# Performance work log

Measured on AMD Instinct MI355X. Metric: run time of the kernel, lower is better.

Reference implementation:

```python
import jax, jax.numpy as jnp
import numpy as np


def setup_inputs() -> dict:
    key = jax.random.key(0)
    ks = jax.random.split(key, 7)
    E = 768; CH = 3; PS = 16; B = 128; P = 196
    return {
        "x": jax.random.normal(ks[0], (B, P, E), dtype=jnp.float32),
        "We": jax.random.normal(ks[1], (CH * PS * PS, E), dtype=jnp.float32) * (1.0 / np.sqrt(E)),
        "be": jax.random.normal(ks[2], (CH * PS * PS,), dtype=jnp.float32) * 0.01,
        "filter_re": jax.random.normal(ks[3], (1, 1, 1, PS, PS), dtype=jnp.float32),
        "filter_im": jax.random.normal(ks[4], (1, 1, 1, PS, PS), dtype=jnp.float32),
        "Wd": jax.random.normal(ks[5], (E, CH * PS * PS), dtype=jnp.float32) * (1.0 / np.sqrt(CH * PS * PS)),
        "bd": jax.random.normal(ks[6], (E,), dtype=jnp.float32) * 0.01,
        "ch": 3,
        "patch_size": 16,
    }


def reference(x, We, be, filter_re, filter_im, Wd, bd, ch, patch_size):
    # encode: [b,p,E] -> [b,p,ch*ps*ps]
    h = jnp.einsum('bpe,ce->bpc', x, We) + be
    b, p, _ = h.shape
    h = h.reshape(b, p, ch, patch_size, patch_size)
    # batched 2D FFT over the two trailing patch dims
    hf = jnp.fft.fft2(h, axes=(-2, -1))
    filt = (filter_re + 1j * filter_im).astype(hf.dtype)  # [1,1,1,ps,ps]
    r = jnp.fft.ifft2(hf * filt, axes=(-2, -1))
    a = jnp.abs(r).reshape(b, p, ch * patch_size * patch_size)
    # decode: [b,p,ch*ps*ps] -> [b,p,E]
    return jnp.einsum('bpc,ec->bpe', a, Wd) + bd
```

## Files before the change

kernel.cpp:

```cpp
#include <hip/hip_runtime.h>

typedef short short8 __attribute__((ext_vector_type(8)));
typedef unsigned short ushort8 __attribute__((ext_vector_type(8)));
typedef float f32x4 __attribute__((ext_vector_type(4)));

__device__ __forceinline__ unsigned short f32_to_bf16(float f) {
  unsigned u = __float_as_uint(f);
  unsigned r = 0x7fffu + ((u >> 16) & 1u);
  return (unsigned short)((u + r) >> 16);
}

__global__ void cvt_f32_bf16(const float* __restrict__ s,
                             unsigned short* __restrict__ d, int n8) {
  int i = blockIdx.x * blockDim.x + threadIdx.x;
  if (i >= n8) return;
  const float4* sp = (const float4*)s;
  float4 a = sp[2 * i], b = sp[2 * i + 1];
  ushort8 o;
  o[0] = f32_to_bf16(a.x); o[1] = f32_to_bf16(a.y);
  o[2] = f32_to_bf16(a.z); o[3] = f32_to_bf16(a.w);
  o[4] = f32_to_bf16(b.x); o[5] = f32_to_bf16(b.y);
  o[6] = f32_to_bf16(b.z); o[7] = f32_to_bf16(b.w);
  ((ushort8*)d)[i] = o;
}

__device__ __forceinline__ void gload_lds16(const void* g, void* l) {
  auto* gp = (const __attribute__((address_space(1))) uint32_t*)((uintptr_t)g);
  auto* lp = (__attribute__((address_space(3))) uint32_t*)(uint32_t)(uintptr_t)l;
  __builtin_amdgcn_global_load_lds(gp, lp, 16, 0, 0);
}

constexpr float C16T[16] = {
    1.f,  0.9238795325112867f,  0.7071067811865476f,  0.3826834323650898f,
    0.f, -0.3826834323650898f, -0.7071067811865476f, -0.9238795325112867f,
   -1.f, -0.9238795325112867f, -0.7071067811865476f, -0.3826834323650898f,
    0.f,  0.3826834323650898f,  0.7071067811865476f,  0.9238795325112867f};
constexpr float S16T[16] = {
    0.f,  0.3826834323650898f,  0.7071067811865476f,  0.9238795325112867f,
    1.f,  0.9238795325112867f,  0.7071067811865476f,  0.3826834323650898f,
    0.f, -0.3826834323650898f, -0.7071067811865476f, -0.9238795325112867f,
   -1.f, -0.9238795325112867f, -0.7071067811865476f, -0.3826834323650898f};

__global__ __launch_bounds__(256) void build_gpp(
    const float* __restrict__ fre, const float* __restrict__ fim,
    unsigned short* __restrict__ Gpp) {
  __shared__ float Gr[256], Gi[256];
  const int t = threadIdx.x;
  const int d1 = t >> 4, d2 = t & 15;
  float sr = 0.f, si = 0.f;
#pragma unroll
  for (int v1 = 0; v1 < 16; ++v1) {
    const int k1 = (v1 * d1) & 15;
#pragma unroll
    for (int v2 = 0; v2 < 16; ++v2) {
      const int k = (k1 + v2 * d2) & 15;
      const float c = C16T[k], s = S16T[k];
      const float a = fre[v1 * 16 + v2], b = fim[v1 * 16 + v2];
      sr += a * c - b * s;
      si += a * s + b * c;
    }
  }
  Gr[t] = sr * (1.f / 256.f);
  Gi[t] = si * (1.f / 256.f);
  __syncthreads();
  const int p = blockIdx.x;
  const int p1 = p >> 4, p2 = p & 15;
  const size_t rre = (size_t)(p >> 5) * 64 + (p & 31);
  const int q1 = t >> 4, q2 = t & 15;
  const int idx = (((p1 - q1) & 15) << 4) | ((p2 - q2) & 15);
  Gpp[rre * 256 + t] = f32_to_bf16(Gr[idx]);
  Gpp[(rre + 32) * 256 + t] = f32_to_bf16(Gi[idx]);
}

template <int MODE>
__global__ __launch_bounds__(256, 5) void gemm32(
    const unsigned short* __restrict__ A, const unsigned short* __restrict__ B,
    const float* __restrict__ bias, void* __restrict__ out,
    int M, int K, int nbx, int ldo) {
  __shared__ __align__(16) unsigned short As[2][128 * 32];
  __shared__ __align__(16) unsigned short Bs[2][128 * 32];

  const int tid = threadIdx.x;
  const int lane = tid & 63;
  const int wid = tid >> 6;
  const int wr = wid >> 1, wc = wid & 1;

  const int nwg = gridDim.x;
  const int cpx = nwg >> 3;
  const int bid = blockIdx.x;
  const int lid = (bid & 7) * cpx + (bid >> 3);
  const int m0 = (lid / nbx) * 128, n0 = (lid % nbx) * 128;

  const int srow = tid >> 2;
  const int sgo = (((tid & 3) ^ ((tid >> 3) & 3)) << 3);
  char* AsC = (char*)&As[0][0];
  char* BsC = (char*)&Bs[0][0];

  auto STAGE = [&](int buf, int kt) {
    const int k0 = kt * 32 + sgo;
#pragma unroll
    for (int l = 0; l < 2; ++l) {
      gload_lds16(A + (size_t)(m0 + l * 64 + srow) * K + k0,
                  AsC + buf * 8192 + l * 4096 + (wid << 10));
      gload_lds16(B + (size_t)(n0 + l * 64 + srow) * K + k0,
                  BsC + buf * 8192 + l * 4096 + (wid << 10));
    }
  };

  const int rsel = lane & 15;
  const int kslot = ((lane >> 4) ^ ((lane >> 1) & 3)) << 4;

  f32x4 acc[4][4] = {};

  auto COMPUTE = [&](int buf) {
    const char* Ab = AsC + buf * 8192;
    const char* Bb = BsC + buf * 8192;
    short8 af[4], bf[4];
#pragma unroll
    for (int m = 0; m < 4; ++m)
      af[m] = *(const short8*)(Ab + (wr * 64 + m * 16 + rsel) * 64 + kslot);
#pragma unroll
    for (int n = 0; n < 4; ++n)
      bf[n] = *(const short8*)(Bb + (wc * 64 + n * 16 + rsel) * 64 + kslot);
#pragma unroll
    for (int m = 0; m < 4; ++m)
#pragma unroll
      for (int n = 0; n < 4; ++n)
        acc[m][n] = __builtin_amdgcn_mfma_f32_16x16x32_bf16(
            af[m], bf[n], acc[m][n], 0, 0, 0);
  };

  const int nk = K >> 5;
  STAGE(0, 0);
  __syncthreads();
  int cur = 0;
  for (int t = 1; t < nk; ++t) {
    STAGE(cur ^ 1, t);
    COMPUTE(cur);
    __syncthreads();
    cur ^= 1;
  }
  COMPUTE(cur);

  const int fr = lane & 15, fq = lane >> 4;
  if (MODE == 2) {
    const int cbase = (n0 + wc * 64) >> 1;
    unsigned short* o = (unsigned short*)out;
#pragma unroll
    for (int n = 0; n < 2; ++n) {
      const int gcol = cbase + n * 16 + fr;
#pragma unroll
      for (int m = 0; m < 4; ++m) {
        const int grow = m0 + wr * 64 + m * 16 + fq * 4;
#pragma unroll
        for (int j = 0; j < 4; ++j) {
          const float re = acc[m][n][j];
          const float im = acc[m][n + 2][j];
          o[(size_t)(grow + j) * ldo + gcol] =
              f32_to_bf16(sqrtf(re * re + im * im));
        }
      }
    }
  } else {
#pragma unroll
    for (int n = 0; n < 4; ++n) {
      const int gcol = n0 + wc * 64 + n * 16 + fr;
      const float bv = bias[gcol];
#pragma unroll
      for (int m = 0; m < 4; ++m) {
        const int grow = m0 + wr * 64 + m * 16 + fq * 4;
#pragma unroll
        for (int j = 0; j < 4; ++j) {
          const float v = acc[m][n][j] + bv;
          if (MODE == 1)
            ((unsigned short*)out)[(size_t)(grow + j) * ldo + gcol] =
                f32_to_bf16(v);
          else
            ((float*)out)[(size_t)(grow + j) * ldo + gcol] = v;
        }
      }
    }
  }
}

extern "C" void kernel_launch(void* const* d_in, const int* in_sizes, int n_in,
                              void* d_out, int out_size, void* d_ws,
                              size_t ws_size, hipStream_t stream) {
  const float* x   = (const float*)d_in[0];
  const float* We  = (const float*)d_in[1];
  const float* be  = (const float*)d_in[2];
  const float* fre = (const float*)d_in[3];
  const float* fim = (const float*)d_in[4];
  const float* Wd  = (const float*)d_in[5];
  const float* bd  = (const float*)d_in[6];

  const int E = 768, C = 768;
  const int nX = in_sizes[0];
  const int M  = nX / E;
  const int nW = E * C;

  char* w = (char*)d_ws;
  unsigned short* xb  = (unsigned short*)w;
  unsigned short* Web = (unsigned short*)(w + (size_t)nX * 2);
  unsigned short* Wdb = Web + nW;
  unsigned short* Gpp = Wdb + nW;
  unsigned short* hb  = Gpp + 512 * 256;

  cvt_f32_bf16<<<(nX / 8 + 255) / 256, 256, 0, stream>>>(x, xb, nX / 8);
  cvt_f32_bf16<<<(nW / 8 + 255) / 256, 256, 0, stream>>>(We, Web, nW / 8);
  cvt_f32_bf16<<<(nW / 8 + 255) / 256, 256, 0, stream>>>(Wd, Wdb, nW / 8);

  build_gpp<<<256, 256, 0, stream>>>(fre, fim, Gpp);

  gemm32<1><<<6 * (M / 128), 256, 0, stream>>>(xb, Web, be, hb, M, E, 6, 768);

  const int M2 = M * 3;
  gemm32<2><<<4 * (M2 / 128), 256, 0, stream>>>(hb, Gpp, nullptr, xb, M2, 256,
                                                4, 256);

  gemm32<0><<<6 * (M / 128), 256, 0, stream>>>(xb, Wdb, bd, (float*)d_out, M,
                                               C, 6, 768);
}
```

Before: 185.2 us.

## Deepen GEMM K-tile to 64 with vmcnt-based double-buffer pipeline

The shared GEMM kernel now stages 64-wide K tiles instead of 32, using an XOR swizzle on 128-byte LDS rows. The main loop now issues two stages up front and waits on vmcnt counts with raw barriers rather than __syncthreads, so global-to-LDS loads for tile t+2 overlap compute on tile t. The aim is fewer barriers per K step and more latency hiding. LDS use doubles to 64KB per block, and the launch-bounds occupancy hint is dropped, which may reduce resident blocks.

```diff
diff --git a/kernel.cpp b/kernel.cpp
--- a/kernel.cpp
+++ b/kernel.cpp
@@ -30,6 +30,20 @@
   __builtin_amdgcn_global_load_lds(gp, lp, 16, 0, 0);
 }
 
+#define WAIT8()                                        \
+  do {                                                 \
+    asm volatile("s_waitcnt vmcnt(8)" ::: "memory");   \
+  } while (0)
+#define WAIT0()                                        \
+  do {                                                 \
+    asm volatile("s_waitcnt vmcnt(0)" ::: "memory");   \
+  } while (0)
+#define BAR()                                          \
+  do {                                                 \
+    __builtin_amdgcn_s_barrier();                      \
+    __builtin_amdgcn_sched_barrier(0);                 \
+  } while (0)
+
 constexpr float C16T[16] = {
     1.f,  0.9238795325112867f,  0.7071067811865476f,  0.3826834323650898f,
     0.f, -0.3826834323650898f, -0.7071067811865476f, -0.9238795325112867f,
@@ -73,12 +87,12 @@
 }
 
 template <int MODE>
-__global__ __launch_bounds__(256, 5) void gemm32(
+__global__ __launch_bounds__(256) void gemm_cv(
     const unsigned short* __restrict__ A, const unsigned short* __restrict__ B,
     const float* __restrict__ bias, void* __restrict__ out,
     int M, int K, int nbx, int ldo) {
-  __shared__ __align__(16) unsigned short As[2][128 * 32];
-  __shared__ __align__(16) unsigned short Bs[2][128 * 32];
+  __shared__ __align__(16) unsigned short As[2][128 * 64];
+  __shared__ __align__(16) unsigned short Bs[2][128 * 64];
 
   const int tid = threadIdx.x;
   const int lane = tid & 63;
@@ -91,56 +105,59 @@
   const int lid = (bid & 7) * cpx + (bid >> 3);
   const int m0 = (lid / nbx) * 128, n0 = (lid % nbx) * 128;
 
-  const int srow = tid >> 2;
-  const int sgo = (((tid & 3) ^ ((tid >> 3) & 3)) << 3);
-  char* AsC = (char*)&As[0][0];
-  char* BsC = (char*)&Bs[0][0];
+  const int lr8 = lane >> 3;
+  const int swk = ((lane & 7) ^ lr8) * 8;
+
+  f32x4 acc[4][4] = {};
 
   auto STAGE = [&](int buf, int kt) {
-    const int k0 = kt * 32 + sgo;
-#pragma unroll
-    for (int l = 0; l < 2; ++l) {
-      gload_lds16(A + (size_t)(m0 + l * 64 + srow) * K + k0,
-                  AsC + buf * 8192 + l * 4096 + (wid << 10));
-      gload_lds16(B + (size_t)(n0 + l * 64 + srow) * K + k0,
-                  BsC + buf * 8192 + l * 4096 + (wid << 10));
+    const int k0 = kt * 64 + swk;
+#pragma unroll
+    for (int c = 0; c < 4; ++c) {
+      const int rowc = wid * 32 + c * 8;
+      gload_lds16(A + (size_t)(m0 + rowc + lr8) * K + k0, &As[buf][rowc * 64]);
+      gload_lds16(B + (size_t)(n0 + rowc + lr8) * K + k0, &Bs[buf][rowc * 64]);
     }
   };
 
   const int rsel = lane & 15;
-  const int kslot = ((lane >> 4) ^ ((lane >> 1) & 3)) << 4;
-
-  f32x4 acc[4][4] = {};
-
   auto COMPUTE = [&](int buf) {
-    const char* Ab = AsC + buf * 8192;
-    const char* Bb = BsC + buf * 8192;
-    short8 af[4], bf[4];
-#pragma unroll
-    for (int m = 0; m < 4; ++m)
-      af[m] = *(const short8*)(Ab + (wr * 64 + m * 16 + rsel) * 64 + kslot);
-#pragma unroll
-    for (int n = 0; n < 4; ++n)
-      bf[n] = *(const short8*)(Bb + (wc * 64 + n * 16 + rsel) * 64 + kslot);
-#pragma unroll
-    for (int m = 0; m < 4; ++m)
-#pragma unroll
-      for (int n = 0; n < 4; ++n)
-        acc[m][n] = __builtin_amdgcn_mfma_f32_16x16x32_bf16(
-            af[m], bf[n], acc[m][n], 0, 0, 0);
+#pragma unroll
+    for (int ks = 0; ks < 2; ++ks) {
+      const int kbyte = ks * 64 + (lane >> 4) * 16;
+      short8 af[4], bf[4];
+#pragma unroll
+      for (int m = 0; m < 4; ++m) {
+        const int row = wr * 64 + m * 16 + rsel;
+        af[m] = *(const short8*)((const char*)&As[buf][0] +
+                                 row * 128 + (kbyte ^ ((row & 7) << 4)));
+      }
+#pragma unroll
+      for (int n = 0; n < 4; ++n) {
+        const int row = wc * 64 + n * 16 + rsel;
+        bf[n] = *(const short8*)((const char*)&Bs[buf][0] +
+                                 row * 128 + (kbyte ^ ((row & 7) << 4)));
+      }
+#pragma unroll
+      for (int m = 0; m < 4; ++m)
+#pragma unroll
+        for (int n = 0; n < 4; ++n)
+          acc[m][n] = __builtin_amdgcn_mfma_f32_16x16x32_bf16(
+              af[m], bf[n], acc[m][n], 0, 0, 0);
+    }
   };
 
-  const int nk = K >> 5;
+  const int nk = K >> 6;
   STAGE(0, 0);
-  __syncthreads();
-  int cur = 0;
-  for (int t = 1; t < nk; ++t) {
-    STAGE(cur ^ 1, t);
-    COMPUTE(cur);
-    __syncthreads();
-    cur ^= 1;
+  STAGE(1, 1);
+  for (int t = 0; t < nk; ++t) {
+    if (t + 1 < nk) WAIT8();
+    else            WAIT0();
+    BAR();
+    COMPUTE(t & 1);
+    __builtin_amdgcn_s_barrier();
+    if (t + 2 < nk) STAGE(t & 1, t + 2);
   }
-  COMPUTE(cur);
 
   const int fr = lane & 15, fq = lane >> 4;
   if (MODE == 2) {
@@ -212,12 +229,12 @@
 
   build_gpp<<<256, 256, 0, stream>>>(fre, fim, Gpp);
 
-  gemm32<1><<<6 * (M / 128), 256, 0, stream>>>(xb, Web, be, hb, M, E, 6, 768);
+  gemm_cv<1><<<6 * (M / 128), 256, 0, stream>>>(xb, Web, be, hb, M, E, 6, 768);
 
   const int M2 = M * 3;
-  gemm32<2><<<4 * (M2 / 128), 256, 0, stream>>>(hb, Gpp, nullptr, xb, M2, 256,
-                                                4, 256);
-
-  gemm32<0><<<6 * (M / 128), 256, 0, stream>>>(xb, Wdb, bd, (float*)d_out, M,
-                                               C, 6, 768);
-}
+  gemm_cv<2><<<4 * (M2 / 128), 256, 0, stream>>>(hb, Gpp, nullptr, xb, M2, 256,
+                                                 4, 256);
+
+  gemm_cv<0><<<6 * (M / 128), 256, 0, stream>>>(xb, Wdb, bd, (float*)d_out, M,
+                                                C, 6, 768);
+}
```

Result: faster. 153.4 us (-17.2%).
